# Kernel tuning notes

Measured on AMD Instinct MI355X. Metric: run time of the kernel, lower is better.

Reference implementation:

```python
import jax, jax.numpy as jnp
import numpy as np

_THR = 0.008856  # OpenCV Lab threshold (6/29)^3


def _f_lab(t):
    # f(t) = t^(1/3) if t > thr else 7.787*t + 16/116 ; safe-where avoids nan/inf grads at 0
    safe = jnp.where(t > _THR, t, 1.0)
    return jnp.where(t > _THR, jnp.cbrt(safe), 7.787 * t + 16.0 / 116.0)


def _rgb_to_lab(img):
    """img: [B,3,H,W] in [0,1] -> OpenCV 8-bit-scaled Lab, divided by 255 (as in the torch code)."""
    img = jnp.clip(img, 0.0, 1.0)  # blur mixes channels so values can exceed 1; cv2 path saturates to 8-bit range
    r, g, b = img[:, 0], img[:, 1], img[:, 2]
    # linear RGB -> XYZ (OpenCV matrix), with white-point normalization of X and Z
    X = (0.412453 * r + 0.357580 * g + 0.180423 * b) / 0.950456
    Y = 0.212671 * r + 0.715160 * g + 0.072169 * b
    Z = (0.019334 * r + 0.119193 * g + 0.950227 * b) / 1.088754
    fX, fY, fZ = _f_lab(X), _f_lab(Y), _f_lab(Z)
    safeY = jnp.where(Y > _THR, Y, 1.0)
    L = jnp.where(Y > _THR, 116.0 * jnp.cbrt(safeY) - 16.0, 903.3 * Y)
    a = 500.0 * (fX - fY) + 128.0
    bb = 200.0 * (fY - fZ) + 128.0
    # OpenCV 8-bit scaling: L*255/100, a+128, b+128 ; torch code then divides by 255
    lab = jnp.stack([L * 255.0 / 100.0, a, bb], axis=1) / 255.0
    return lab


def _blur(img, weight):
    # F.conv2d with ones(3,3,5,5)/25, padding=2: each output channel is the SUM over input
    # channels of the 5x5 mean (full channel mixing, as in the torch module).
    return jax.lax.conv_general_dilated(
        img, weight, window_strides=(1, 1), padding=[(2, 2), (2, 2)],
        dimension_numbers=("NCHW", "OIHW", "NCHW"))


def setup_inputs() -> dict:
    key = jax.random.key(0)
    k1, k2 = jax.random.split(key)
    B, C, H, W = 32, 3, 512, 512
    img1 = jax.random.uniform(k1, (B, C, H, W), dtype=jnp.float32)
    img2 = jax.random.uniform(k2, (B, C, H, W), dtype=jnp.float32)
    kernel_size = 5
    weight = jnp.ones((3, 3, kernel_size, kernel_size), dtype=jnp.float32) / (kernel_size ** 2)
    return {"img1": img1, "img2": img2, "weight": weight}


def reference(img1, img2, weight):
    lab1 = _rgb_to_lab(_blur(img1, weight))
    lab2 = _rgb_to_lab(_blur(img2, weight))
    return jnp.mean((lab1 - lab2) ** 2)  # F.mse_loss, reduction='mean'
```

## Files before the change

kernel.cpp:

```cpp
#include <hip/hip_runtime.h>


constexpr int TILE  = 64;
constexpr int HALO  = 2;
constexpr int ROWS  = TILE + 2 * HALO;
constexpr int CPAD  = 72;
constexpr int NF4   = CPAD / 4;
constexpr int NITER = ROWS * NF4;
constexpr int IMG_H = 512;
constexpr int IMG_W = 512;
constexpr int BATCH = 32;
constexpr int NBLOCKS = 1024;
constexpr float THR = 0.008856f;

__device__ __forceinline__ void issue_loads(const float* __restrict__ base,
                                            int by0, int bx0, int tid,
                                            float4 rv[5], float4 gv[5], float4 bv[5])
{
    const size_t plane = (size_t)IMG_H * IMG_W;
    #pragma unroll
    for (int k = 0; k < 5; ++k) {
        int n    = tid + 256 * k;
        int row  = n / NF4;
        int col4 = (n - row * NF4) * 4;
        int gy   = by0 + row - HALO;
        int gx   = bx0 + col4 - 4;
        float4 z = make_float4(0.f, 0.f, 0.f, 0.f);
        rv[k] = z; gv[k] = z; bv[k] = z;
        if (n < NITER && (unsigned)gy < (unsigned)IMG_H && (unsigned)gx < (unsigned)IMG_W) {
            const float* p = base + (size_t)gy * IMG_W + gx;
            rv[k] = *(const float4*)(p);
            gv[k] = *(const float4*)(p + plane);
            bv[k] = *(const float4*)(p + 2 * plane);
        }
    }
}

__device__ __forceinline__ void write_stage(float* __restrict__ buf, int tid,
                                            const float4 rv[5], const float4 gv[5],
                                            const float4 bv[5])
{
    #pragma unroll
    for (int k = 0; k < 5; ++k) {
        int n = tid + 256 * k;
        if (n < NITER) {
            int row  = n / NF4;
            int col4 = (n - row * NF4) * 4;
            float4 v;
            v.x = rv[k].x + gv[k].x + bv[k].x;
            v.y = rv[k].y + gv[k].y + bv[k].y;
            v.z = rv[k].z + gv[k].z + bv[k].z;
            v.w = rv[k].w + gv[k].w + bv[k].w;
            *(float4*)&buf[row * CPAD + col4] = v;
        }
    }
}

__device__ __forceinline__ void compute_unit(const float* __restrict__ buf,
                                             int x, int r0, float wtap, bool first,
                                             float L1[16], float& acc)
{
    const float* colbase = buf + x + 2;
    float h0 = colbase[(r0    ) * CPAD] + colbase[(r0    ) * CPAD + 1] + colbase[(r0    ) * CPAD + 2] + colbase[(r0    ) * CPAD + 3] + colbase[(r0    ) * CPAD + 4];
    float h1 = colbase[(r0 + 1) * CPAD] + colbase[(r0 + 1) * CPAD + 1] + colbase[(r0 + 1) * CPAD + 2] + colbase[(r0 + 1) * CPAD + 3] + colbase[(r0 + 1) * CPAD + 4];
    float h2 = colbase[(r0 + 2) * CPAD] + colbase[(r0 + 2) * CPAD + 1] + colbase[(r0 + 2) * CPAD + 2] + colbase[(r0 + 2) * CPAD + 3] + colbase[(r0 + 2) * CPAD + 4];
    float h3 = colbase[(r0 + 3) * CPAD] + colbase[(r0 + 3) * CPAD + 1] + colbase[(r0 + 3) * CPAD + 2] + colbase[(r0 + 3) * CPAD + 3] + colbase[(r0 + 3) * CPAD + 4];
    #pragma unroll
    for (int k = 0; k < 16; ++k) {
        const float* p = colbase + (r0 + 4 + k) * CPAD;
        float h4 = p[0] + p[1] + p[2] + p[3] + p[4];
        float v  = (h0 + h1 + h2 + h3 + h4) * wtap;
        v = fminf(fmaxf(v, 0.f), 1.f);
        float L = (v > THR) ? (116.f * cbrtf(v) - 16.f) : (903.3f * v);
        if (first) L1[k] = L;
        else { float d = L1[k] - L; acc += d * d; }
        h0 = h1; h1 = h2; h2 = h3; h3 = h4;
    }
}

__global__ __launch_bounds__(256, 4)
void lcol_mse_kernel(const float* __restrict__ img1,
                     const float* __restrict__ img2,
                     const float* __restrict__ weight,
                     float* __restrict__ out)
{
    __shared__ float cs[2][ROWS * CPAD];
    __shared__ float wpart[4];

    const int tid = threadIdx.x;
    const int x   = tid & 63;
    const int r0  = (tid >> 6) * 16;
    const float wtap = weight[0];
    const size_t plane = (size_t)IMG_H * IMG_W;

    int by0s[2], bx0s[2];
    const float* bases[4];
    #pragma unroll
    for (int t = 0; t < 2; ++t) {
        int tile = (int)blockIdx.x + t * NBLOCKS;
        int b    = tile >> 6;
        int rem  = tile & 63;
        by0s[t]  = (rem >> 3) * TILE;
        bx0s[t]  = (rem & 7) * TILE;
        bases[2 * t]     = img1 + (size_t)b * 3 * plane;
        bases[2 * t + 1] = img2 + (size_t)b * 3 * plane;
    }

    float L1[16];
    float acc = 0.f;
    float4 rv[5], gv[5], bv[5];

    issue_loads(bases[0], by0s[0], bx0s[0], tid, rv, gv, bv);
    write_stage(cs[0], tid, rv, gv, bv);
    __syncthreads();

    #pragma unroll
    for (int u = 0; u < 4; ++u) {
        if (u < 3)
            issue_loads(bases[u + 1], by0s[(u + 1) >> 1], bx0s[(u + 1) >> 1],
                        tid, rv, gv, bv);
        compute_unit(cs[u & 1], x, r0, wtap, (u & 1) == 0, L1, acc);
        if (u < 3)
            write_stage(cs[(u + 1) & 1], tid, rv, gv, bv);
        __syncthreads();
    }

    #pragma unroll
    for (int off = 32; off; off >>= 1) acc += __shfl_down(acc, off);
    if ((tid & 63) == 0) wpart[tid >> 6] = acc;
    __syncthreads();
    if (tid == 0) {
        float s = wpart[0] + wpart[1] + wpart[2] + wpart[3];
        const float scale = (float)(1.0 / (10000.0 * (double)BATCH * 3.0 * IMG_H * IMG_W));
        atomicAdd(out, s * scale);
    }
}

extern "C" void kernel_launch(void* const* d_in, const int* in_sizes, int n_in,
                              void* d_out, int out_size, void* d_ws, size_t ws_size,
                              hipStream_t stream) {
    const float* img1   = (const float*)d_in[0];
    const float* img2   = (const float*)d_in[1];
    const float* weight = (const float*)d_in[2];
    float* out = (float*)d_out;

    hipMemsetAsync(out, 0, sizeof(float), stream);

    lcol_mse_kernel<<<dim3(NBLOCKS), dim3(256), 0, stream>>>(img1, img2, weight, out);
}
```

Before: 228.5 us.

## Use one tile per block and a separate deterministic reduction kernel

Each block now handles a single tile pair (2048 blocks) instead of two tiles per block with a four-stage pipeline. Per-block partial sums go to a workspace, and a second single-block kernel reduces them, replacing the memset plus atomicAdd. This gives more blocks for latency hiding and drops the atomic, but loses the cross-tile load/compute overlap and adds a kernel launch.

```diff
diff --git a/kernel.cpp b/kernel.cpp
--- a/kernel.cpp
+++ b/kernel.cpp
@@ -10,7 +10,7 @@
 constexpr int IMG_H = 512;
 constexpr int IMG_W = 512;
 constexpr int BATCH = 32;
-constexpr int NBLOCKS = 1024;
+constexpr int NTILES = 2048;
 constexpr float THR = 0.008856f;
 
 __device__ __forceinline__ void issue_loads(const float* __restrict__ base,
@@ -82,7 +82,7 @@
 void lcol_mse_kernel(const float* __restrict__ img1,
                      const float* __restrict__ img2,
                      const float* __restrict__ weight,
-                     float* __restrict__ out)
+                     float* __restrict__ part)
 {
     __shared__ float cs[2][ROWS * CPAD];
     __shared__ float wpart[4];
@@ -93,46 +93,52 @@
     const float wtap = weight[0];
     const size_t plane = (size_t)IMG_H * IMG_W;
 
-    int by0s[2], bx0s[2];
-    const float* bases[4];
-    #pragma unroll
-    for (int t = 0; t < 2; ++t) {
-        int tile = (int)blockIdx.x + t * NBLOCKS;
-        int b    = tile >> 6;
-        int rem  = tile & 63;
-        by0s[t]  = (rem >> 3) * TILE;
-        bx0s[t]  = (rem & 7) * TILE;
-        bases[2 * t]     = img1 + (size_t)b * 3 * plane;
-        bases[2 * t + 1] = img2 + (size_t)b * 3 * plane;
-    }
+    const int tile = (int)blockIdx.x;
+    const int b    = tile >> 6;
+    const int rem  = tile & 63;
+    const int by0  = (rem >> 3) * TILE;
+    const int bx0  = (rem & 7) * TILE;
+    const float* base1 = img1 + (size_t)b * 3 * plane;
+    const float* base2 = img2 + (size_t)b * 3 * plane;
 
     float L1[16];
     float acc = 0.f;
     float4 rv[5], gv[5], bv[5];
 
-    issue_loads(bases[0], by0s[0], bx0s[0], tid, rv, gv, bv);
+    issue_loads(base1, by0, bx0, tid, rv, gv, bv);
     write_stage(cs[0], tid, rv, gv, bv);
     __syncthreads();
 
-    #pragma unroll
-    for (int u = 0; u < 4; ++u) {
-        if (u < 3)
-            issue_loads(bases[u + 1], by0s[(u + 1) >> 1], bx0s[(u + 1) >> 1],
-                        tid, rv, gv, bv);
-        compute_unit(cs[u & 1], x, r0, wtap, (u & 1) == 0, L1, acc);
-        if (u < 3)
-            write_stage(cs[(u + 1) & 1], tid, rv, gv, bv);
-        __syncthreads();
-    }
+    issue_loads(base2, by0, bx0, tid, rv, gv, bv);
+    compute_unit(cs[0], x, r0, wtap, true, L1, acc);
+    write_stage(cs[1], tid, rv, gv, bv);
+    __syncthreads();
+
+    compute_unit(cs[1], x, r0, wtap, false, L1, acc);
 
     #pragma unroll
     for (int off = 32; off; off >>= 1) acc += __shfl_down(acc, off);
     if ((tid & 63) == 0) wpart[tid >> 6] = acc;
     __syncthreads();
+    if (tid == 0)
+        part[tile] = wpart[0] + wpart[1] + wpart[2] + wpart[3];
+}
+
+__global__ __launch_bounds__(256)
+void lcol_reduce_kernel(const float* __restrict__ part, float* __restrict__ out)
+{
+    __shared__ float w[4];
+    const int tid = threadIdx.x;
+    float s = 0.f;
+    #pragma unroll
+    for (int k = 0; k < NTILES / 256; ++k) s += part[tid + 256 * k];
+    #pragma unroll
+    for (int off = 32; off; off >>= 1) s += __shfl_down(s, off);
+    if ((tid & 63) == 0) w[tid >> 6] = s;
+    __syncthreads();
     if (tid == 0) {
-        float s = wpart[0] + wpart[1] + wpart[2] + wpart[3];
         const float scale = (float)(1.0 / (10000.0 * (double)BATCH * 3.0 * IMG_H * IMG_W));
-        atomicAdd(out, s * scale);
+        out[0] = (w[0] + w[1] + w[2] + w[3]) * scale;
     }
 }
 
@@ -142,9 +148,9 @@
     const float* img1   = (const float*)d_in[0];
     const float* img2   = (const float*)d_in[1];
     const float* weight = (const float*)d_in[2];
-    float* out = (float*)d_out;
+    float* out  = (float*)d_out;
+    float* part = (float*)d_ws;
 
-    hipMemsetAsync(out, 0, sizeof(float), stream);
-
-    lcol_mse_kernel<<<dim3(NBLOCKS), dim3(256), 0, stream>>>(img1, img2, weight, out);
+    lcol_mse_kernel<<<dim3(NTILES), dim3(256), 0, stream>>>(img1, img2, weight, part);
+    lcol_reduce_kernel<<<dim3(1), dim3(256), 0, stream>>>(part, out);
 }
```

After: 222.1 us. 1.03x faster.
